# Performance work log

Hardware: AMD Instinct MI355X
Metric: run time of the kernel (lower is better)

## Reference

```python
import jax, jax.numpy as jnp
import numpy as np

EPS = 1e-12

def _l2norm(v):
    return v / jnp.maximum(jnp.linalg.norm(v), EPS)

def setup_inputs() -> dict:
    key = jax.random.key(0)
    k1, k2, k3, k4 = jax.random.split(key, 4)
    B, C, H, Wd = 32, 64, 128, 128
    x = jax.random.normal(k1, (B, C, H, Wd), dtype=jnp.float32)
    W = jax.random.normal(k2, (C, C), dtype=jnp.float32)
    gamma = jax.random.uniform(k3, (1,), dtype=jnp.float32)
    u = jax.random.normal(k4, (C,), dtype=jnp.float32)
    return {"x": x, "W": W, "gamma": gamma, "u": u}

def reference(x, W, gamma, u):
    # --- spectral norm: one power iteration (u is the stored buffer) ---
    v = _l2norm(W.T @ u)          # [C]
    u2 = _l2norm(W @ v)           # [C]
    sigma = u2 @ (W @ v)          # scalar, largest singular value estimate
    Wsn = W / sigma               # ks=1 conv weight, normalized

    B, C = x.shape[0], x.shape[1]
    xf = x.reshape(B, C, -1)                        # [B,C,N]
    convx = jnp.einsum('oc,bcn->bon', Wsn, xf)      # 1x1 conv
    xxT = jnp.einsum('bcn,bdn->bcd', xf, xf)        # Gram [B,C,C]
    o = jnp.einsum('bcd,bdn->bcn', xxT, convx)      # [B,C,N]
    out = gamma[0] * o + xf
    return out.reshape(x.shape)
```

## Files before the change

### kernel.cpp

```cpp
#include <hip/hip_runtime.h>

#define NN 16384
#define CC 64
#define BB 32

typedef __attribute__((ext_vector_type(8))) short bf16x8;
typedef __attribute__((ext_vector_type(4))) short bf16x4;
typedef __attribute__((ext_vector_type(4))) float f32x4;
typedef __attribute__((ext_vector_type(16))) float f32x16;

__device__ __forceinline__ unsigned short f2bf(float f) {
    unsigned int u = __float_as_uint(f);
    unsigned int r = (u + 0x7fffu + ((u >> 16) & 1u)) >> 16;
    return (unsigned short)r;
}

__device__ __forceinline__ bf16x8 cvt8(float4 a, float4 b) {
    union { bf16x8 v; unsigned short s[8]; } u;
    u.s[0] = f2bf(a.x); u.s[1] = f2bf(a.y); u.s[2] = f2bf(a.z); u.s[3] = f2bf(a.w);
    u.s[4] = f2bf(b.x); u.s[5] = f2bf(b.y); u.s[6] = f2bf(b.z); u.s[7] = f2bf(b.w);
    return u.v;
}

#define GP 68
__global__ __launch_bounds__(512) void k_gram(const float* __restrict__ x,
                                              float* __restrict__ Gp,
                                              unsigned short* __restrict__ Xbf) {
    int b = blockIdx.x >> 3, chunk = blockIdx.x & 7;
    int wave = threadIdx.x >> 6, lane = threadIdx.x & 63;
    int lrow = lane & 15, quad = lane >> 4;
    const float* xb = x + (size_t)b * CC * NN;
    unsigned short* xo = Xbf + (size_t)b * CC * NN;
    int kbase = chunk * 2048 + wave * 256;

    __shared__ float Gw[8 * 64 * GP];

    f32x4 acc[4][4] = {};
    for (int ks = 0; ks < 8; ++ks) {
        int k0 = kbase + ks * 32 + quad * 8;
        bf16x8 fr[4];
        #pragma unroll
        for (int ti = 0; ti < 4; ++ti) {
            const float* p = xb + (size_t)(16 * ti + lrow) * NN + k0;
            float4 a  = *(const float4*)p;
            float4 b4 = *(const float4*)(p + 4);
            fr[ti] = cvt8(a, b4);
        }
        #pragma unroll
        for (int ti = 0; ti < 4; ++ti)
            *(bf16x8*)(xo + (size_t)(16 * ti + lrow) * NN + k0) = fr[ti];
        #pragma unroll
        for (int mi = 0; mi < 4; ++mi)
            #pragma unroll
            for (int ni = 0; ni < 4; ++ni)
                acc[mi][ni] = __builtin_amdgcn_mfma_f32_16x16x32_bf16(
                    fr[mi], fr[ni], acc[mi][ni], 0, 0, 0);
    }

    float* gw = Gw + wave * 64 * GP;
    #pragma unroll
    for (int mi = 0; mi < 4; ++mi)
        #pragma unroll
        for (int ni = 0; ni < 4; ++ni)
            #pragma unroll
            for (int r = 0; r < 4; ++r) {
                int row = 16 * mi + quad * 4 + r;
                int col = 16 * ni + lrow;
                gw[row * GP + col] = acc[mi][ni][r];
            }
    __syncthreads();

    float* gp = Gp + ((size_t)b * 8 + chunk) * 4096;
    for (int i = threadIdx.x; i < 4096; i += 512) {
        int off = (i >> 6) * GP + (i & 63);
        float s = 0.f;
        #pragma unroll
        for (int w = 0; w < 8; ++w) s += Gw[w * 64 * GP + off];
        gp[i] = s;
    }
}

__global__ __launch_bounds__(256) void k_build_A(const float* __restrict__ W,
                                                 const float* __restrict__ u,
                                                 const float* __restrict__ gamma,
                                                 const float* __restrict__ Gp,
                                                 unsigned short* __restrict__ Afrag) {
    int b = blockIdx.x;
    int tid = threadIdx.x;
    __shared__ float Ws[4096];
    __shared__ float Gs[64 * 65];
    __shared__ float As[64 * 68];
    __shared__ float us[64];
    __shared__ float gshare;

    for (int i = tid; i < 4096; i += 256) Ws[i] = W[i];
    if (tid < 64) us[tid] = u[tid];
    __syncthreads();

    if (tid < 64) {
        int c = tid;
        float t = 0.f;
        #pragma unroll 8
        for (int r = 0; r < 64; ++r) t += Ws[r * 64 + c] * us[r];
        float s = t * t;
        #pragma unroll
        for (int m = 1; m < 64; m <<= 1) s += __shfl_xor(s, m);
        float v = t / fmaxf(sqrtf(s), 1e-12f);
        float wv = 0.f;
        #pragma unroll 8
        for (int k = 0; k < 64; ++k) wv += Ws[c * 64 + k] * __shfl(v, k);
        float s2 = wv * wv;
        #pragma unroll
        for (int m = 1; m < 64; m <<= 1) s2 += __shfl_xor(s2, m);
        float nw = sqrtf(s2);
        float sigma = s2 / fmaxf(nw, 1e-12f);
        if (c == 0) gshare = gamma[0] / fmaxf(sigma, 1e-30f);
    }

    const float* gp = Gp + (size_t)b * 8 * 4096;
    for (int i = tid; i < 4096; i += 256) {
        float s = 0.f;
        #pragma unroll
        for (int c = 0; c < 8; ++c) s += gp[c * 4096 + i];
        Gs[(i >> 6) * 65 + (i & 63)] = s;
    }
    __syncthreads();

    {
        int r = tid >> 2, j0 = (tid & 3) * 16;
        float a[16];
        #pragma unroll
        for (int j = 0; j < 16; ++j) a[j] = 0.f;
        for (int k = 0; k < 64; ++k) {
            float g = Gs[r * 65 + k];
            const float* wr = &Ws[k * 64 + j0];
            float4 w0 = *(const float4*)(wr);
            float4 w1 = *(const float4*)(wr + 4);
            float4 w2 = *(const float4*)(wr + 8);
            float4 w3 = *(const float4*)(wr + 12);
            a[0]  += g * w0.x; a[1]  += g * w0.y; a[2]  += g * w0.z; a[3]  += g * w0.w;
            a[4]  += g * w1.x; a[5]  += g * w1.y; a[6]  += g * w1.z; a[7]  += g * w1.w;
            a[8]  += g * w2.x; a[9]  += g * w2.y; a[10] += g * w2.z; a[11] += g * w2.w;
            a[12] += g * w3.x; a[13] += g * w3.y; a[14] += g * w3.z; a[15] += g * w3.w;
        }
        float g2 = gshare;
        #pragma unroll
        for (int j = 0; j < 16; ++j) {
            float vv = a[j] * g2 + ((r == j0 + j) ? 1.f : 0.f);
            As[r * 68 + j0 + j] = vv;
        }
    }
    __syncthreads();

    unsigned short* Ab = Afrag + (size_t)b * 4096;
    for (int fv = tid; fv < 512; fv += 256) {
        int ks = fv >> 7, mi = (fv >> 6) & 1, lane = fv & 63;
        int row = 32 * mi + (lane & 31);
        int col = 16 * ks + (lane >> 5) * 8;
        float4 a4 = *(const float4*)&As[row * 68 + col];
        float4 b4 = *(const float4*)&As[row * 68 + col + 4];
        *(bf16x8*)(Ab + (size_t)fv * 8) = cvt8(a4, b4);
    }
}

#define PITCH 68
__global__ __launch_bounds__(256) void k_out(const unsigned short* __restrict__ Xbf,
                                             const unsigned short* __restrict__ Afrag,
                                             float* __restrict__ out) {
    int nblk = blockIdx.x & 127;
    int b = blockIdx.x >> 7;
    int col0 = nblk * 128;
    int wave = threadIdx.x >> 6, lane = threadIdx.x & 63;
    const unsigned short* xb = Xbf + (size_t)b * CC * NN;

    __shared__ __align__(16) unsigned short XT[128 * PITCH];

    {
        int rp = threadIdx.x & 31;
        int nc = threadIdx.x >> 5;
        int r0 = rp * 2;
        int cs = nc * 16;
        const unsigned short* pr0 = xb + (size_t)r0 * NN + col0 + cs;
        const unsigned short* pr1 = pr0 + NN;
        union { bf16x8 v; unsigned short s[8]; } a0, a1, b0, b1;
        a0.v = *(const bf16x8*)(pr0);
        a1.v = *(const bf16x8*)(pr0 + 8);
        b0.v = *(const bf16x8*)(pr1);
        b1.v = *(const bf16x8*)(pr1 + 8);
        #pragma unroll
        for (int e = 0; e < 8; ++e) {
            *(unsigned int*)&XT[(cs + e) * PITCH + r0] =
                (unsigned)a0.s[e] | ((unsigned)b0.s[e] << 16);
            *(unsigned int*)&XT[(cs + 8 + e) * PITCH + r0] =
                (unsigned)a1.s[e] | ((unsigned)b1.s[e] << 16);
        }
    }

    bf16x8 af[4][2];
    const unsigned short* Ab = Afrag + (size_t)b * 4096;
    #pragma unroll
    for (int ks = 0; ks < 4; ++ks)
        #pragma unroll
        for (int mi = 0; mi < 2; ++mi)
            af[ks][mi] = *(const bf16x8*)(Ab + ((ks * 2 + mi) * 64 + lane) * 8);

    __syncthreads();

    f32x16 acc[2] = {};
    int n = wave * 32 + (lane & 31);
    int kh = (lane >> 5) * 8;
    #pragma unroll
    for (int ks = 0; ks < 4; ++ks) {
        union { bf16x8 v; bf16x4 h[2]; } bu;
        bu.h[0] = *(const bf16x4*)&XT[n * PITCH + ks * 16 + kh];
        bu.h[1] = *(const bf16x4*)&XT[n * PITCH + ks * 16 + kh + 4];
        acc[0] = __builtin_amdgcn_mfma_f32_32x32x16_bf16(af[ks][0], bu.v, acc[0], 0, 0, 0);
        acc[1] = __builtin_amdgcn_mfma_f32_32x32x16_bf16(af[ks][1], bu.v, acc[1], 0, 0, 0);
    }

    float* ob = out + (size_t)b * CC * NN;
    int gcol = col0 + n;
    #pragma unroll
    for (int mi = 0; mi < 2; ++mi)
        #pragma unroll
        for (int r = 0; r < 16; ++r) {
            int grow = 32 * mi + (r & 3) + 8 * (r >> 2) + 4 * (lane >> 5);
            ob[(size_t)grow * NN + gcol] = acc[mi][r];
        }
}

extern "C" void kernel_launch(void* const* d_in, const int* in_sizes, int n_in,
                              void* d_out, int out_size, void* d_ws, size_t ws_size,
                              hipStream_t stream) {
    const float* x     = (const float*)d_in[0];
    const float* W     = (const float*)d_in[1];
    const float* gamma = (const float*)d_in[2];
    const float* u     = (const float*)d_in[3];
    float* out = (float*)d_out;

    char* ws = (char*)d_ws;
    float* Gp             = (float*)ws;
    unsigned short* Afrag = (unsigned short*)(ws + (5 << 20));
    unsigned short* Xbf   = (unsigned short*)(ws + (6 << 20));

    k_gram<<<BB * 8, 512, 0, stream>>>(x, Gp, Xbf);
    k_build_A<<<BB, 256, 0, stream>>>(W, u, gamma, Gp, Afrag);
    k_out<<<BB * 128, 256, 0, stream>>>(Xbf, Afrag, out);
}
```

Before: 306.4 us.

## Restructure Gram kernel with LDS double-buffered staging and more chunks per batch

The Gram kernel now splits each batch into 32 chunks instead of 8. Each block loads fp32 tiles with coalesced float4 reads, converts them to bf16, and stages them in a double-buffered LDS tile while also writing the bf16 copy out. Each wave computes a 16x32 slice of the 64x64 Gram block, which removes the per-wave 64x64 accumulators and the LDS cross-wave reduction. The cost is more partial Gram matrices that k_build_A must sum (32 per batch), a larger workspace layout, and extra barriers.

```diff
diff --git a/kernel.cpp b/kernel.cpp
--- a/kernel.cpp
+++ b/kernel.cpp
@@ -3,6 +3,10 @@
 #define NN 16384
 #define CC 64
 #define BB 32
+#define NCH 32
+#define CHUNK 512
+#define KSTAGE 128
+#define XP 136
 
 typedef __attribute__((ext_vector_type(8))) short bf16x8;
 typedef __attribute__((ext_vector_type(4))) short bf16x4;
@@ -22,62 +26,87 @@
     return u.v;
 }
 
-#define GP 68
-__global__ __launch_bounds__(512) void k_gram(const float* __restrict__ x,
-                                              float* __restrict__ Gp,
-                                              unsigned short* __restrict__ Xbf) {
-    int b = blockIdx.x >> 3, chunk = blockIdx.x & 7;
-    int wave = threadIdx.x >> 6, lane = threadIdx.x & 63;
-    int lrow = lane & 15, quad = lane >> 4;
+__global__ __launch_bounds__(512, 6) void k_gram(const float* __restrict__ x,
+                                                 float* __restrict__ Gp,
+                                                 unsigned short* __restrict__ Xbf) {
+    const int b = blockIdx.x >> 5, chunk = blockIdx.x & 31;
+    const int t = threadIdx.x;
+    const int lane = t & 63;
+    const int lrow = lane & 15, quad = lane >> 4;
+    const int wave = t >> 6;
+    const int mi = wave >> 1, ni0 = (wave & 1) * 2;
+
     const float* xb = x + (size_t)b * CC * NN;
     unsigned short* xo = Xbf + (size_t)b * CC * NN;
-    int kbase = chunk * 2048 + wave * 256;
-
-    __shared__ float Gw[8 * 64 * GP];
-
-    f32x4 acc[4][4] = {};
-    for (int ks = 0; ks < 8; ++ks) {
-        int k0 = kbase + ks * 32 + quad * 8;
-        bf16x8 fr[4];
-        #pragma unroll
-        for (int ti = 0; ti < 4; ++ti) {
-            const float* p = xb + (size_t)(16 * ti + lrow) * NN + k0;
-            float4 a  = *(const float4*)p;
-            float4 b4 = *(const float4*)(p + 4);
-            fr[ti] = cvt8(a, b4);
-        }
-        #pragma unroll
-        for (int ti = 0; ti < 4; ++ti)
-            *(bf16x8*)(xo + (size_t)(16 * ti + lrow) * NN + k0) = fr[ti];
-        #pragma unroll
-        for (int mi = 0; mi < 4; ++mi)
-            #pragma unroll
-            for (int ni = 0; ni < 4; ++ni)
-                acc[mi][ni] = __builtin_amdgcn_mfma_f32_16x16x32_bf16(
-                    fr[mi], fr[ni], acc[mi][ni], 0, 0, 0);
-    }
-
-    float* gw = Gw + wave * 64 * GP;
-    #pragma unroll
-    for (int mi = 0; mi < 4; ++mi)
-        #pragma unroll
-        for (int ni = 0; ni < 4; ++ni)
-            #pragma unroll
-            for (int r = 0; r < 4; ++r) {
-                int row = 16 * mi + quad * 4 + r;
-                int col = 16 * ni + lrow;
-                gw[row * GP + col] = acc[mi][ni][r];
-            }
-    __syncthreads();
-
-    float* gp = Gp + ((size_t)b * 8 + chunk) * 4096;
-    for (int i = threadIdx.x; i < 4096; i += 512) {
-        int off = (i >> 6) * GP + (i & 63);
-        float s = 0.f;
-        #pragma unroll
-        for (int w = 0; w < 8; ++w) s += Gw[w * 64 * GP + off];
-        gp[i] = s;
-    }
+    const int kbase = chunk * CHUNK;
+
+    const int r0 = t >> 5, c4 = t & 31;
+
+    __shared__ __align__(16) unsigned short Xs[2][64 * XP];
+
+    float4 sv0, sv1, sv2, sv3;
+
+#define LOADS(s)                                                                  \
+    {                                                                             \
+        const float* p = xb + kbase + (s) * KSTAGE + c4 * 4;                      \
+        sv0 = *(const float4*)(p + (size_t)(r0)      * NN);                       \
+        sv1 = *(const float4*)(p + (size_t)(r0 + 16) * NN);                       \
+        sv2 = *(const float4*)(p + (size_t)(r0 + 32) * NN);                       \
+        sv3 = *(const float4*)(p + (size_t)(r0 + 48) * NN);                       \
+    }
+
+#define WRITES(s)                                                                 \
+    {                                                                             \
+        unsigned short* bp = &Xs[(s) & 1][0];                                     \
+        const float4 vv[4] = {sv0, sv1, sv2, sv3};                                \
+        _Pragma("unroll")                                                         \
+        for (int i = 0; i < 4; ++i) {                                             \
+            unsigned int lo = (unsigned)f2bf(vv[i].x) | ((unsigned)f2bf(vv[i].y) << 16); \
+            unsigned int hi = (unsigned)f2bf(vv[i].z) | ((unsigned)f2bf(vv[i].w) << 16); \
+            uint2 pk = make_uint2(lo, hi);                                        \
+            *(uint2*)&bp[(r0 + 16 * i) * XP + c4 * 4] = pk;                       \
+            *(uint2*)(xo + (size_t)(r0 + 16 * i) * NN + kbase + (s) * KSTAGE + c4 * 4) = pk; \
+        }                                                                         \
+    }
+
+    f32x4 acc0 = {}, acc1 = {};
+
+#define COMPUTE(s)                                                                \
+    {                                                                             \
+        const unsigned short* bp = &Xs[(s) & 1][0];                               \
+        _Pragma("unroll")                                                         \
+        for (int ks = 0; ks < 4; ++ks) {                                          \
+            int kcol = ks * 32 + quad * 8;                                        \
+            bf16x8 fa  = *(const bf16x8*)&bp[(16 * mi        + lrow) * XP + kcol];\
+            bf16x8 fb0 = *(const bf16x8*)&bp[(16 * ni0       + lrow) * XP + kcol];\
+            bf16x8 fb1 = *(const bf16x8*)&bp[(16 * (ni0 + 1) + lrow) * XP + kcol];\
+            acc0 = __builtin_amdgcn_mfma_f32_16x16x32_bf16(fa, fb0, acc0, 0, 0, 0);\
+            acc1 = __builtin_amdgcn_mfma_f32_16x16x32_bf16(fa, fb1, acc1, 0, 0, 0);\
+        }                                                                         \
+    }
+
+    LOADS(0);
+    WRITES(0);
+    __syncthreads();
+
+    #pragma unroll
+    for (int s = 0; s < 4; ++s) {
+        if (s < 3) LOADS(s + 1);
+        COMPUTE(s);
+        if (s < 3) WRITES(s + 1);
+        __syncthreads();
+    }
+
+    float* gp = Gp + ((size_t)b * NCH + chunk) * 4096;
+    #pragma unroll
+    for (int r = 0; r < 4; ++r) {
+        int row = 16 * mi + quad * 4 + r;
+        gp[row * 64 + 16 * ni0 + lrow]        = acc0[r];
+        gp[row * 64 + 16 * (ni0 + 1) + lrow]  = acc1[r];
+    }
+#undef LOADS
+#undef WRITES
+#undef COMPUTE
 }
 
 __global__ __launch_bounds__(256) void k_build_A(const float* __restrict__ W,
@@ -117,11 +146,11 @@
         if (c == 0) gshare = gamma[0] / fmaxf(sigma, 1e-30f);
     }
 
-    const float* gp = Gp + (size_t)b * 8 * 4096;
+    const float* gp = Gp + (size_t)b * NCH * 4096;
     for (int i = tid; i < 4096; i += 256) {
         float s = 0.f;
         #pragma unroll
-        for (int c = 0; c < 8; ++c) s += gp[c * 4096 + i];
+        for (int c = 0; c < NCH; ++c) s += gp[c * 4096 + i];
         Gs[(i >> 6) * 65 + (i & 63)] = s;
     }
     __syncthreads();
@@ -240,10 +269,10 @@
 
     char* ws = (char*)d_ws;
     float* Gp             = (float*)ws;
-    unsigned short* Afrag = (unsigned short*)(ws + (5 << 20));
-    unsigned short* Xbf   = (unsigned short*)(ws + (6 << 20));
-
-    k_gram<<<BB * 8, 512, 0, stream>>>(x, Gp, Xbf);
+    unsigned short* Afrag = (unsigned short*)(ws + (16 << 20));
+    unsigned short* Xbf   = (unsigned short*)(ws + (17 << 20));
+
+    k_gram<<<BB * NCH, 512, 0, stream>>>(x, Gp, Xbf);
     k_build_A<<<BB, 256, 0, stream>>>(W, u, gamma, Gp, Afrag);
     k_out<<<BB * 128, 256, 0, stream>>>(Xbf, Afrag, out);
 }
```

Result: faster. 287.5 us (-6.2%).
